# Performance work log

Hardware: AMD Instinct MI355X
Metric: run time of the kernel (lower is better)

Reference implementation:

```python
import jax, jax.numpy as jnp
import numpy as np

N = 50000
E = 1600000
IN_CH = 34
HID = 64
OUT = 64
NEG_SLOPE = 0.2


def _gat_layer(x, src, dst, W, a_src, a_dst, bias, heads, out_ch, concat):
    n = x.shape[0]
    xw = (x @ W).reshape(n, heads, out_ch)                      # [N,H,C]
    al_src = jnp.sum(xw * a_src[None], axis=-1)                  # [N,H]
    al_dst = jnp.sum(xw * a_dst[None], axis=-1)                  # [N,H]
    e = jax.nn.leaky_relu(al_src[src] + al_dst[dst], NEG_SLOPE)  # [E,H]
    # segment softmax over incoming edges of each dst node (self-loops ensure non-empty)
    m = jax.ops.segment_max(e, dst, num_segments=n)              # [N,H]
    ex = jnp.exp(e - m[dst])
    denom = jax.ops.segment_sum(ex, dst, num_segments=n)         # [N,H]
    alpha = ex / denom[dst]                                      # [E,H]
    msg = xw[src] * alpha[:, :, None]                            # [E,H,C]
    out = jax.ops.segment_sum(msg, dst, num_segments=n)          # [N,H,C]
    if concat:
        out = out.reshape(n, heads * out_ch)
    else:
        out = out.mean(axis=1)
    return out + bias


def setup_inputs() -> dict:
    key = jax.random.key(0)
    ks = jax.random.split(key, 12)
    x = jax.random.normal(ks[0], (N, IN_CH), dtype=jnp.float32)
    edge_index = jax.random.randint(ks[1], (2, E), 0, N, dtype=jnp.int64)
    # layer 1: heads=2, concat -> 128
    W1 = jax.random.normal(ks[2], (IN_CH, 2 * HID), dtype=jnp.float32) * 0.1
    a_src1 = jax.random.normal(ks[3], (2, HID), dtype=jnp.float32) * 0.1
    a_dst1 = jax.random.normal(ks[4], (2, HID), dtype=jnp.float32) * 0.1
    b1 = jnp.zeros((2 * HID,), dtype=jnp.float32)
    # layer 2: heads=1, mean
    W2 = jax.random.normal(ks[5], (2 * HID, OUT), dtype=jnp.float32) * 0.1
    a_src2 = jax.random.normal(ks[6], (1, OUT), dtype=jnp.float32) * 0.1
    a_dst2 = jax.random.normal(ks[7], (1, OUT), dtype=jnp.float32) * 0.1
    b2 = jnp.zeros((OUT,), dtype=jnp.float32)
    return {"x": x, "edge_index": edge_index, "W1": W1, "a_src1": a_src1,
            "a_dst1": a_dst1, "b1": b1, "W2": W2, "a_src2": a_src2,
            "a_dst2": a_dst2, "b2": b2}


def reference(x, edge_index, W1, a_src1, a_dst1, b1, W2, a_src2, a_dst2, b2):
    n = x.shape[0]
    loops = jnp.arange(n, dtype=edge_index.dtype)
    src = jnp.concatenate([edge_index[0], loops])  # PyG GATConv add_self_loops=True
    dst = jnp.concatenate([edge_index[1], loops])
    h = _gat_layer(x, src, dst, W1, a_src1, a_dst1, b1, heads=2, out_ch=HID, concat=True)
    h = jax.nn.relu(h)
    out = _gat_layer(h, src, dst, W2, a_src2, a_dst2, b2, heads=1, out_ch=OUT, concat=False)
    return out
```

## Files before the change

### kernel.cpp

```cpp
#include <hip/hip_runtime.h>
#include <math.h>

#define N_NODES 50000
#define E_EDGES 1600000
#define IN_CH   34
#define NEG     0.2f
#define NB      196
#define CAP     10000

typedef __attribute__((ext_vector_type(2))) float fv2;

static __device__ __forceinline__ unsigned short f2bf(float f) {
    unsigned int u = __float_as_uint(f);
    u += 0x7fffu + ((u >> 16) & 1u);
    return (unsigned short)(u >> 16);
}
static __device__ __forceinline__ float bflo(unsigned int u) {
    return __uint_as_float(u << 16);
}
static __device__ __forceinline__ float bfhi(unsigned int u) {
    return __uint_as_float(u & 0xffff0000u);
}
static __device__ __forceinline__ float lrelu_exp(float e) {
    return expf(e > 0.f ? e : NEG * e);
}

static __device__ __forceinline__ int scan256_excl(int v, int* wsum) {
    const int lane = threadIdx.x & 63, wv = threadIdx.x >> 6;
    int x = v;
    #pragma unroll
    for (int off = 1; off < 64; off <<= 1) {
        int y = __shfl_up(x, off);
        if (lane >= off) x += y;
    }
    if (lane == 63) wsum[wv] = x;
    __syncthreads();
    if (threadIdx.x < 4) {
        int s = wsum[threadIdx.x];
        #pragma unroll
        for (int off = 1; off < 4; off <<= 1) {
            int y = __shfl_up(s, off);
            if ((int)threadIdx.x >= off) s += y;
        }
        wsum[threadIdx.x] = s;
    }
    __syncthreads();
    const int woff = wv ? wsum[wv - 1] : 0;
    return woff + x - v;
}

__global__ __launch_bounds__(256) void k_bin_node1(
    const int* __restrict__ srcA, const int* __restrict__ dstA,
    int* __restrict__ gcur, unsigned int* __restrict__ binned,
    const float* __restrict__ x, const float* __restrict__ W1,
    const float* __restrict__ a_src, const float* __restrict__ a_dst,
    unsigned short* __restrict__ xw1b,
    float* __restrict__ al_s, float* __restrict__ al_d)
{
    __shared__ __align__(16) char sm[69664];
    const int tid = threadIdx.x;

    if (blockIdx.x < NB) {
        unsigned int* raw  = (unsigned int*)sm;
        unsigned int* ebuf = (unsigned int*)(sm + 32768);
        int* cnt  = (int*)(sm + 65536);
        int* loff = (int*)(sm + 66560);
        int* lcur = (int*)(sm + 67584);
        int* cur  = (int*)(sm + 68608);
        int* wsum = (int*)(sm + 69632);
        cnt[tid] = 0;
        __syncthreads();
        const int base = blockIdx.x * 8192;
        #pragma unroll
        for (int i = 0; i < 32; ++i) {
            const int e = base + i * 256 + tid;
            if (e < E_EDGES) {
                const int d = dstA[e], s = srcA[e];
                raw[i * 256 + tid] = ((unsigned int)d << 16) | (unsigned int)s;
                atomicAdd(&cnt[d >> 8], 1);
            }
        }
        __syncthreads();
        const int v = cnt[tid];
        const int excl = scan256_excl(v, wsum);
        loff[tid] = excl;
        lcur[tid] = excl;
        cur[tid] = (tid < NB && v > 0) ? (tid * CAP + atomicAdd(&gcur[tid], v)) : 0;
        __syncthreads();
        const int mE = min(8192, E_EDGES - base);
        #pragma unroll
        for (int i = 0; i < 32; ++i) {
            const int p = i * 256 + tid;
            if (p < mE) {
                const unsigned int u = raw[p];
                const int q = atomicAdd(&lcur[u >> 24], 1);
                ebuf[q] = u;
            }
        }
        __syncthreads();
        #pragma unroll
        for (int i = 0; i < 32; ++i) {
            const int p = i * 256 + tid;
            if (p < mE) {
                const unsigned int u = ebuf[p];
                const int b = (int)(u >> 24);
                binned[cur[b] + (p - loff[b])] = u;
            }
        }
    } else {
        float* sW  = (float*)sm;
        float* sx  = (float*)(sm + 17952);
        float* sas = (float*)(sm + 22432);
        float* sad = (float*)(sm + 22944);
        for (int i = tid; i < IN_CH * 128; i += 256) {
            int k = i >> 7, c = i & 127;
            sW[k * 132 + c] = W1[i];
        }
        if (tid < 128) { sas[tid] = a_src[tid]; sad[tid] = a_dst[tid]; }
        const int n0 = (blockIdx.x - NB) * 32;
        for (int i = tid; i < 32 * IN_CH; i += 256) {
            int n = i / IN_CH;
            sx[n * 35 + (i - n * IN_CH)] = (n0 + n < N_NODES) ? x[n0 * IN_CH + i] : 0.f;
        }
        __syncthreads();

        const int tc = tid & 31, tn = tid >> 5;
        float acc[4][4] = {{0.f}};
        for (int k = 0; k < IN_CH; ++k) {
            const float4 wv = *reinterpret_cast<const float4*>(&sW[k * 132 + 4 * tc]);
            #pragma unroll
            for (int j = 0; j < 4; ++j) {
                const float hj = sx[(4 * tn + j) * 35 + k];
                acc[j][0] += hj * wv.x; acc[j][1] += hj * wv.y;
                acc[j][2] += hj * wv.z; acc[j][3] += hj * wv.w;
            }
        }
        #pragma unroll
        for (int j = 0; j < 4; ++j) {
            const int node = n0 + 4 * tn + j;
            float ps = 0.f, pd = 0.f;
            #pragma unroll
            for (int c = 0; c < 4; ++c) {
                ps += acc[j][c] * sas[4 * tc + c];
                pd += acc[j][c] * sad[4 * tc + c];
            }
            #pragma unroll
            for (int off = 1; off < 16; off <<= 1) {
                ps += __shfl_xor(ps, off);
                pd += __shfl_xor(pd, off);
            }
            if (node < N_NODES) {
                if ((tc & 15) == 0) {
                    int h = tc >> 4;
                    al_s[node * 2 + h] = ps;
                    al_d[node * 2 + h] = pd;
                }
                ushort4 u;
                u.x = f2bf(acc[j][0]); u.y = f2bf(acc[j][1]);
                u.z = f2bf(acc[j][2]); u.w = f2bf(acc[j][3]);
                *reinterpret_cast<ushort4*>(&xw1b[node * 128 + 4 * tc]) = u;
            }
        }
    }
}

__global__ __launch_bounds__(256) void k_fine(
    const int* __restrict__ gcur, const unsigned int* __restrict__ binned,
    int2* __restrict__ rowspan, int* __restrict__ sorted_src)
{
    __shared__ unsigned int sbin[CAP];
    __shared__ int cnt[256], lcur[256];
    __shared__ int wsum[4];
    const int tid = threadIdx.x;
    const int b = blockIdx.x;
    const int bbase = b * CAP;
    const int cntb = gcur[b];
    cnt[tid] = 0;
    __syncthreads();
    for (int p = tid; p < cntb; p += 256) {
        const unsigned int u = binned[bbase + p];
        sbin[p] = u;
        atomicAdd(&cnt[(u >> 16) & 255], 1);
    }
    __syncthreads();
    const int v = cnt[tid];
    const int excl = scan256_excl(v, wsum);
    const int node = b * 256 + tid;
    if (node < N_NODES) rowspan[node] = make_int2(bbase + excl, bbase + excl + v);
    lcur[tid] = excl;
    __syncthreads();
    for (int p = tid; p < cntb; p += 256) {
        const unsigned int u = sbin[p];
        const int q = atomicAdd(&lcur[(u >> 16) & 255], 1);
        sorted_src[bbase + q] = (int)(u & 0xffffu);
    }
}

__global__ __launch_bounds__(256) void k_gather1(
    const int2* __restrict__ rowspan, const int* __restrict__ sorted_src,
    const unsigned int* __restrict__ xw1u,
    const float* __restrict__ al_s, const float* __restrict__ al_d,
    const float* __restrict__ b1, float* __restrict__ hbuf)
{
    __shared__ float4 AB[2][4][32];
    const int wave = threadIdx.x >> 6;
    const int lane = threadIdx.x & 63;
    const int node = (blockIdx.x * 256 + threadIdx.x) >> 6;
    if (node >= N_NODES) return;
    const int2 span = rowspan[node];
    const int head = lane >> 5;

    const float2 ald  = *reinterpret_cast<const float2*>(&al_d[node * 2]);
    const float2 als0 = *reinterpret_cast<const float2*>(&al_s[node * 2]);
    const float w0h0 = lrelu_exp(als0.x + ald.x);
    const float w0h1 = lrelu_exp(als0.y + ald.y);
    const float wself = head ? w0h1 : w0h0;

    const unsigned int su = xw1u[node * 64 + lane];
    fv2 accX = { wself * bflo(su), wself * bfhi(su) };
    fv2 accY = { 0.f, 0.f };
    float dv0 = 0.f, dv1 = 0.f;
    const float4* ABh = AB[head][wave];

    for (int base = span.x; base < span.y; base += 64) {
        const int rem = span.y - base;
        const int m = rem < 64 ? rem : 64;
        const int mp = (m + 1) & ~1;
        if (lane < m) {
            const int s = sorted_src[base + lane];
            const float2 als = *reinterpret_cast<const float2*>(&al_s[s * 2]);
            const float w0 = lrelu_exp(als.x + ald.x);
            const float w1 = lrelu_exp(als.y + ald.y);
            dv0 += w0; dv1 += w1;
            const float offf = __int_as_float(s << 6);
            ((float2*)&AB[0][wave][lane >> 1])[lane & 1] = make_float2(offf, w0);
            ((float2*)&AB[1][wave][lane >> 1])[lane & 1] = make_float2(offf, w1);
        } else if (lane < mp) {
            const float offf = __int_as_float(node << 6);
            ((float2*)&AB[0][wave][lane >> 1])[lane & 1] = make_float2(offf, 0.f);
            ((float2*)&AB[1][wave][lane >> 1])[lane & 1] = make_float2(offf, 0.f);
        }
        const int P = mp >> 1;
        int p = 0;
        for (; p + 4 <= P; p += 4) {
            const float4 q0 = ABh[p + 0];
            const float4 q1 = ABh[p + 1];
            const float4 q2 = ABh[p + 2];
            const float4 q3 = ABh[p + 3];
            const unsigned int a0 = xw1u[__float_as_int(q0.x) + lane];
            const unsigned int b0 = xw1u[__float_as_int(q0.z) + lane];
            const unsigned int a1 = xw1u[__float_as_int(q1.x) + lane];
            const unsigned int b1v = xw1u[__float_as_int(q1.z) + lane];
            const unsigned int a2 = xw1u[__float_as_int(q2.x) + lane];
            const unsigned int b2 = xw1u[__float_as_int(q2.z) + lane];
            const unsigned int a3 = xw1u[__float_as_int(q3.x) + lane];
            const unsigned int b3 = xw1u[__float_as_int(q3.z) + lane];
            fv2 f;
            f.x = bflo(a0); f.y = bfhi(a0); accX += f * q0.y;
            f.x = bflo(b0); f.y = bfhi(b0); accY += f * q0.w;
            f.x = bflo(a1); f.y = bfhi(a1); accX += f * q1.y;
            f.x = bflo(b1v); f.y = bfhi(b1v); accY += f * q1.w;
            f.x = bflo(a2); f.y = bfhi(a2); accX += f * q2.y;
            f.x = bflo(b2); f.y = bfhi(b2); accY += f * q2.w;
            f.x = bflo(a3); f.y = bfhi(a3); accX += f * q3.y;
            f.x = bflo(b3); f.y = bfhi(b3); accY += f * q3.w;
        }
        for (; p < P; ++p) {
            const float4 q = ABh[p];
            const unsigned int a = xw1u[__float_as_int(q.x) + lane];
            const unsigned int b = xw1u[__float_as_int(q.z) + lane];
            fv2 f;
            f.x = bflo(a); f.y = bfhi(a); accX += f * q.y;
            f.x = bflo(b); f.y = bfhi(b); accY += f * q.w;
        }
    }
    accX += accY;
    #pragma unroll
    for (int off = 32; off; off >>= 1) {
        dv0 += __shfl_xor(dv0, off);
        dv1 += __shfl_xor(dv1, off);
    }
    const float den = head ? (dv1 + w0h1) : (dv0 + w0h0);
    const float2 bv = *reinterpret_cast<const float2*>(&b1[2 * lane]);
    float o0 = accX.x / den + bv.x;
    float o1 = accX.y / den + bv.y;
    o0 = o0 > 0.f ? o0 : 0.f;
    o1 = o1 > 0.f ? o1 : 0.f;
    *reinterpret_cast<float2*>(&hbuf[node * 128 + 2 * lane]) = make_float2(o0, o1);
}

__global__ __launch_bounds__(256) void k_node2(
    const float* __restrict__ hbuf, const float* __restrict__ W2,
    const float* __restrict__ a_src, const float* __restrict__ a_dst,
    unsigned short* __restrict__ xw2b, float* __restrict__ al_s, float* __restrict__ al_d)
{
    __shared__ float sW[128 * 64];
    __shared__ float sh[64 * 129];
    __shared__ float sas[64], sad[64];
    const int tid = threadIdx.x;
    for (int i = tid; i < 128 * 64; i += 256) sW[i] = W2[i];
    if (tid < 64) { sas[tid] = a_src[tid]; sad[tid] = a_dst[tid]; }
    const int n0 = blockIdx.x * 64;
    for (int i = tid; i < 64 * 128; i += 256) {
        int n = i >> 7, c = i & 127;
        sh[n * 129 + c] = (n0 + n < N_NODES) ? hbuf[(long)(n0 + n) * 128 + c] : 0.f;
    }
    __syncthreads();

    const int tc = tid & 15, tn = tid >> 4;
    float acc[4][4] = {{0.f}};
    for (int k = 0; k < 128; ++k) {
        const float4 wv = *reinterpret_cast<const float4*>(&sW[k * 64 + 4 * tc]);
        #pragma unroll
        for (int j = 0; j < 4; ++j) {
            const float hj = sh[(4 * tn + j) * 129 + k];
            acc[j][0] += hj * wv.x; acc[j][1] += hj * wv.y;
            acc[j][2] += hj * wv.z; acc[j][3] += hj * wv.w;
        }
    }
    #pragma unroll
    for (int j = 0; j < 4; ++j) {
        const int node = n0 + 4 * tn + j;
        float ps = 0.f, pd = 0.f;
        #pragma unroll
        for (int c = 0; c < 4; ++c) {
            ps += acc[j][c] * sas[4 * tc + c];
            pd += acc[j][c] * sad[4 * tc + c];
        }
        #pragma unroll
        for (int off = 1; off < 16; off <<= 1) {
            ps += __shfl_xor(ps, off);
            pd += __shfl_xor(pd, off);
        }
        if (node < N_NODES) {
            if (tc == 0) { al_s[node] = ps; al_d[node] = pd; }
            ushort4 u;
            u.x = f2bf(acc[j][0]); u.y = f2bf(acc[j][1]);
            u.z = f2bf(acc[j][2]); u.w = f2bf(acc[j][3]);
            *reinterpret_cast<ushort4*>(&xw2b[node * 64 + 4 * tc]) = u;
        }
    }
}

__global__ __launch_bounds__(256) void k_gather2(
    const int2* __restrict__ rowspan, const int* __restrict__ sorted_src,
    const unsigned int* __restrict__ xw2u,
    const float* __restrict__ al_s, const float* __restrict__ al_d,
    const float* __restrict__ b2, float* __restrict__ out)
{
    __shared__ float4 AB[4][32];
    const int wave = threadIdx.x >> 6;
    const int lane = threadIdx.x & 63;
    const int node = (blockIdx.x * 256 + threadIdx.x) >> 6;
    if (node >= N_NODES) return;
    const int2 span = rowspan[node];
    const int li = lane & 31, hsel = lane >> 5;

    const float ald = al_d[node];
    const float w0s = lrelu_exp(al_s[node] + ald);
    const unsigned int su = xw2u[node * 32 + li];
    const float wself = hsel ? 0.f : w0s;
    fv2 acc = { wself * bflo(su), wself * bfhi(su) };
    float dv = 0.f;
    const float4* ABw = AB[wave];

    for (int base = span.x; base < span.y; base += 64) {
        const int rem = span.y - base;
        const int m = rem < 64 ? rem : 64;
        const int mp = (m + 3) & ~3;
        if (lane < m) {
            const int s = sorted_src[base + lane];
            const float w = lrelu_exp(al_s[s] + ald);
            dv += w;
            ((float2*)&AB[wave][lane >> 1])[lane & 1] =
                make_float2(__int_as_float(s << 5), w);
        } else if (lane < mp) {
            ((float2*)&AB[wave][lane >> 1])[lane & 1] =
                make_float2(__int_as_float(node << 5), 0.f);
        }
        const int P = mp >> 1;
        int p = hsel;
        for (; p + 2 < P; p += 4) {
            const float4 qA = ABw[p];
            const float4 qB = ABw[p + 2];
            const unsigned int aA = xw2u[__float_as_int(qA.x) + li];
            const unsigned int bA = xw2u[__float_as_int(qA.z) + li];
            const unsigned int aB = xw2u[__float_as_int(qB.x) + li];
            const unsigned int bB = xw2u[__float_as_int(qB.z) + li];
            fv2 f;
            f.x = bflo(aA); f.y = bfhi(aA); acc += f * qA.y;
            f.x = bflo(bA); f.y = bfhi(bA); acc += f * qA.w;
            f.x = bflo(aB); f.y = bfhi(aB); acc += f * qB.y;
            f.x = bflo(bB); f.y = bfhi(bB); acc += f * qB.w;
        }
        for (; p < P; p += 2) {
            const float4 q = ABw[p];
            const unsigned int a = xw2u[__float_as_int(q.x) + li];
            const unsigned int b = xw2u[__float_as_int(q.z) + li];
            fv2 f;
            f.x = bflo(a); f.y = bfhi(a); acc += f * q.y;
            f.x = bflo(b); f.y = bfhi(b); acc += f * q.w;
        }
    }
    acc.x += __shfl_xor(acc.x, 32);
    acc.y += __shfl_xor(acc.y, 32);
    #pragma unroll
    for (int off = 32; off; off >>= 1) dv += __shfl_xor(dv, off);
    if (lane < 32) {
        const float den = dv + w0s;
        const float2 bv = *reinterpret_cast<const float2*>(&b2[2 * li]);
        *reinterpret_cast<float2*>(&out[node * 64 + 2 * li]) =
            make_float2(acc.x / den + bv.x, acc.y / den + bv.y);
    }
}

extern "C" void kernel_launch(void* const* d_in, const int* in_sizes, int n_in,
                              void* d_out, int out_size, void* d_ws, size_t ws_size,
                              hipStream_t stream)
{
    const float* x   = (const float*)d_in[0];
    const int*   ei  = (const int*)d_in[1];
    const float* W1  = (const float*)d_in[2];
    const float* as1 = (const float*)d_in[3];
    const float* ad1 = (const float*)d_in[4];
    const float* b1  = (const float*)d_in[5];
    const float* W2  = (const float*)d_in[6];
    const float* as2 = (const float*)d_in[7];
    const float* ad2 = (const float*)d_in[8];
    const float* b2  = (const float*)d_in[9];
    float* out = (float*)d_out;

    const int* srcA = ei;
    const int* dstA = ei + E_EDGES;

    char* ws = (char*)d_ws;
    int2*  rowspan    = (int2*)(ws);
    int*   sorted_src = (int*)(ws + 409600);
    int*   gcur       = (int*)(ws + 8249600);
    float* al_s1      = (float*)(ws + 8251648);
    float* al_d1      = (float*)(ws + 8651648);
    float* al_s2      = (float*)(ws + 9051648);
    float* al_d2      = (float*)(ws + 9251648);
    unsigned short* xw1b = (unsigned short*)(ws + 9451648);
    float* hbuf       = (float*)(ws + 22251648);
    unsigned int* binned = (unsigned int*)hbuf;
    unsigned short* xw2b = (unsigned short*)(ws + 47851648);

    hipMemsetAsync(gcur, 0, NB * sizeof(int), stream);
    hipLaunchKernelGGL(k_bin_node1, dim3(NB + (N_NODES + 31) / 32), dim3(256), 0, stream,
                       srcA, dstA, gcur, binned,
                       x, W1, as1, ad1, xw1b, al_s1, al_d1);
    hipLaunchKernelGGL(k_fine, dim3(NB), dim3(256), 0, stream,
                       gcur, binned, rowspan, sorted_src);
    hipLaunchKernelGGL(k_gather1, dim3((N_NODES + 3) / 4), dim3(256), 0, stream,
                       rowspan, sorted_src, (const unsigned int*)xw1b,
                       al_s1, al_d1, b1, hbuf);
    hipLaunchKernelGGL(k_node2, dim3((N_NODES + 63) / 64), dim3(256), 0, stream,
                       hbuf, W2, as2, ad2, xw2b, al_s2, al_d2);
    hipLaunchKernelGGL(k_gather2, dim3((N_NODES + 3) / 4), dim3(256), 0, stream,
                       rowspan, sorted_src, (const unsigned int*)xw2b,
                       al_s2, al_d2, b2, out);
}
```

Before: 268.2 us.

## Fuse layer-2 projection into gather1, split binning, use ranks and 16-bit source indices

Layer 2's linear projection and attention logits now run inside k_gather1. Each wave multiplies its node's relu output by a bf16-packed W2 held in shared memory, so the fp32 hidden buffer and the separate k_node2 kernel are gone. The binning and fine-sort kernels record per-edge ranks from the counting atomics, which removes the second atomic pass and the local reorder buffer; the binning kernel also moves to smaller 4096-edge blocks and is split from the layer-1 node transform. Sorted source indices shrink to uint16 to cut gather traffic, and W2 in bf16 adds rounding error. Every gather1 block now reloads 16KB of W2 from global memory into shared memory, and the grids assume N is divisible by 4.

```diff
diff --git a/kernel.cpp b/kernel.cpp
--- a/kernel.cpp
+++ b/kernel.cpp
@@ -49,127 +49,44 @@
     return woff + x - v;
 }
 
-__global__ __launch_bounds__(256) void k_bin_node1(
+__global__ __launch_bounds__(256) void k_bin(
     const int* __restrict__ srcA, const int* __restrict__ dstA,
-    int* __restrict__ gcur, unsigned int* __restrict__ binned,
-    const float* __restrict__ x, const float* __restrict__ W1,
-    const float* __restrict__ a_src, const float* __restrict__ a_dst,
-    unsigned short* __restrict__ xw1b,
-    float* __restrict__ al_s, float* __restrict__ al_d)
-{
-    __shared__ __align__(16) char sm[69664];
+    int* __restrict__ gcur, unsigned int* __restrict__ binned)
+{
+    __shared__ unsigned int raw[4096];
+    __shared__ unsigned short rnk[4096];
+    __shared__ int cnt[256], cur[256];
     const int tid = threadIdx.x;
-
-    if (blockIdx.x < NB) {
-        unsigned int* raw  = (unsigned int*)sm;
-        unsigned int* ebuf = (unsigned int*)(sm + 32768);
-        int* cnt  = (int*)(sm + 65536);
-        int* loff = (int*)(sm + 66560);
-        int* lcur = (int*)(sm + 67584);
-        int* cur  = (int*)(sm + 68608);
-        int* wsum = (int*)(sm + 69632);
-        cnt[tid] = 0;
-        __syncthreads();
-        const int base = blockIdx.x * 8192;
-        #pragma unroll
-        for (int i = 0; i < 32; ++i) {
-            const int e = base + i * 256 + tid;
-            if (e < E_EDGES) {
-                const int d = dstA[e], s = srcA[e];
-                raw[i * 256 + tid] = ((unsigned int)d << 16) | (unsigned int)s;
-                atomicAdd(&cnt[d >> 8], 1);
-            }
-        }
-        __syncthreads();
-        const int v = cnt[tid];
-        const int excl = scan256_excl(v, wsum);
-        loff[tid] = excl;
-        lcur[tid] = excl;
-        cur[tid] = (tid < NB && v > 0) ? (tid * CAP + atomicAdd(&gcur[tid], v)) : 0;
-        __syncthreads();
-        const int mE = min(8192, E_EDGES - base);
-        #pragma unroll
-        for (int i = 0; i < 32; ++i) {
-            const int p = i * 256 + tid;
-            if (p < mE) {
-                const unsigned int u = raw[p];
-                const int q = atomicAdd(&lcur[u >> 24], 1);
-                ebuf[q] = u;
-            }
-        }
-        __syncthreads();
-        #pragma unroll
-        for (int i = 0; i < 32; ++i) {
-            const int p = i * 256 + tid;
-            if (p < mE) {
-                const unsigned int u = ebuf[p];
-                const int b = (int)(u >> 24);
-                binned[cur[b] + (p - loff[b])] = u;
-            }
-        }
-    } else {
-        float* sW  = (float*)sm;
-        float* sx  = (float*)(sm + 17952);
-        float* sas = (float*)(sm + 22432);
-        float* sad = (float*)(sm + 22944);
-        for (int i = tid; i < IN_CH * 128; i += 256) {
-            int k = i >> 7, c = i & 127;
-            sW[k * 132 + c] = W1[i];
-        }
-        if (tid < 128) { sas[tid] = a_src[tid]; sad[tid] = a_dst[tid]; }
-        const int n0 = (blockIdx.x - NB) * 32;
-        for (int i = tid; i < 32 * IN_CH; i += 256) {
-            int n = i / IN_CH;
-            sx[n * 35 + (i - n * IN_CH)] = (n0 + n < N_NODES) ? x[n0 * IN_CH + i] : 0.f;
-        }
-        __syncthreads();
-
-        const int tc = tid & 31, tn = tid >> 5;
-        float acc[4][4] = {{0.f}};
-        for (int k = 0; k < IN_CH; ++k) {
-            const float4 wv = *reinterpret_cast<const float4*>(&sW[k * 132 + 4 * tc]);
-            #pragma unroll
-            for (int j = 0; j < 4; ++j) {
-                const float hj = sx[(4 * tn + j) * 35 + k];
-                acc[j][0] += hj * wv.x; acc[j][1] += hj * wv.y;
-                acc[j][2] += hj * wv.z; acc[j][3] += hj * wv.w;
-            }
-        }
-        #pragma unroll
-        for (int j = 0; j < 4; ++j) {
-            const int node = n0 + 4 * tn + j;
-            float ps = 0.f, pd = 0.f;
-            #pragma unroll
-            for (int c = 0; c < 4; ++c) {
-                ps += acc[j][c] * sas[4 * tc + c];
-                pd += acc[j][c] * sad[4 * tc + c];
-            }
-            #pragma unroll
-            for (int off = 1; off < 16; off <<= 1) {
-                ps += __shfl_xor(ps, off);
-                pd += __shfl_xor(pd, off);
-            }
-            if (node < N_NODES) {
-                if ((tc & 15) == 0) {
-                    int h = tc >> 4;
-                    al_s[node * 2 + h] = ps;
-                    al_d[node * 2 + h] = pd;
-                }
-                ushort4 u;
-                u.x = f2bf(acc[j][0]); u.y = f2bf(acc[j][1]);
-                u.z = f2bf(acc[j][2]); u.w = f2bf(acc[j][3]);
-                *reinterpret_cast<ushort4*>(&xw1b[node * 128 + 4 * tc]) = u;
-            }
-        }
+    cnt[tid] = 0;
+    __syncthreads();
+    const int base = blockIdx.x * 4096;
+    #pragma unroll
+    for (int i = 0; i < 16; ++i) {
+        const int e = base + i * 256 + tid;
+        if (e < E_EDGES) {
+            const int d = dstA[e], s = srcA[e];
+            raw[i * 256 + tid] = ((unsigned int)d << 16) | (unsigned int)s;
+            rnk[i * 256 + tid] = (unsigned short)atomicAdd(&cnt[d >> 8], 1);
+        }
+    }
+    __syncthreads();
+    const int v = cnt[tid];
+    cur[tid] = (tid < NB && v > 0) ? (tid * CAP + atomicAdd(&gcur[tid], v)) : 0;
+    __syncthreads();
+    const int mE = min(4096, E_EDGES - base);
+    for (int p = tid; p < mE; p += 256) {
+        const unsigned int u = raw[p];
+        binned[cur[u >> 24] + rnk[p]] = u;
     }
 }
 
 __global__ __launch_bounds__(256) void k_fine(
     const int* __restrict__ gcur, const unsigned int* __restrict__ binned,
-    int2* __restrict__ rowspan, int* __restrict__ sorted_src)
+    int2* __restrict__ rowspan, unsigned short* __restrict__ sorted_src)
 {
     __shared__ unsigned int sbin[CAP];
-    __shared__ int cnt[256], lcur[256];
+    __shared__ unsigned short rnk[CAP];
+    __shared__ int cnt[256], sbase[256];
     __shared__ int wsum[4];
     const int tid = threadIdx.x;
     const int b = blockIdx.x;
@@ -180,33 +97,111 @@
     for (int p = tid; p < cntb; p += 256) {
         const unsigned int u = binned[bbase + p];
         sbin[p] = u;
-        atomicAdd(&cnt[(u >> 16) & 255], 1);
+        rnk[p] = (unsigned short)atomicAdd(&cnt[(u >> 16) & 255], 1);
     }
     __syncthreads();
     const int v = cnt[tid];
     const int excl = scan256_excl(v, wsum);
     const int node = b * 256 + tid;
     if (node < N_NODES) rowspan[node] = make_int2(bbase + excl, bbase + excl + v);
-    lcur[tid] = excl;
+    sbase[tid] = excl;
     __syncthreads();
     for (int p = tid; p < cntb; p += 256) {
         const unsigned int u = sbin[p];
-        const int q = atomicAdd(&lcur[(u >> 16) & 255], 1);
-        sorted_src[bbase + q] = (int)(u & 0xffffu);
+        sorted_src[bbase + sbase[(u >> 16) & 255] + rnk[p]] =
+            (unsigned short)(u & 0xffffu);
+    }
+}
+
+__global__ __launch_bounds__(256) void k_node1(
+    const float* __restrict__ x, const float* __restrict__ W1,
+    const float* __restrict__ a_src, const float* __restrict__ a_dst,
+    unsigned short* __restrict__ xw1b,
+    float* __restrict__ al_s, float* __restrict__ al_d,
+    const float* __restrict__ W2, unsigned int* __restrict__ w2p)
+{
+    __shared__ float sW[IN_CH * 132];
+    __shared__ float sx[32 * 35];
+    __shared__ float sas[128], sad[128];
+    const int tid = threadIdx.x;
+    if (blockIdx.x == 0) {
+        for (int i = tid; i < 4096; i += 256) {
+            const int k2 = i >> 6, c = i & 63;
+            const unsigned int lo = f2bf(W2[(2 * k2) * 64 + c]);
+            const unsigned int hi = f2bf(W2[(2 * k2 + 1) * 64 + c]);
+            w2p[i] = lo | (hi << 16);
+        }
+    }
+    for (int i = tid; i < IN_CH * 128; i += 256) {
+        int k = i >> 7, c = i & 127;
+        sW[k * 132 + c] = W1[i];
+    }
+    if (tid < 128) { sas[tid] = a_src[tid]; sad[tid] = a_dst[tid]; }
+    const int n0 = blockIdx.x * 32;
+    for (int i = tid; i < 32 * IN_CH; i += 256) {
+        int n = i / IN_CH;
+        sx[n * 35 + (i - n * IN_CH)] = (n0 + n < N_NODES) ? x[n0 * IN_CH + i] : 0.f;
+    }
+    __syncthreads();
+
+    const int tc = tid & 31, tn = tid >> 5;
+    float acc[4][4] = {{0.f}};
+    for (int k = 0; k < IN_CH; ++k) {
+        const float4 wv = *reinterpret_cast<const float4*>(&sW[k * 132 + 4 * tc]);
+        #pragma unroll
+        for (int j = 0; j < 4; ++j) {
+            const float hj = sx[(4 * tn + j) * 35 + k];
+            acc[j][0] += hj * wv.x; acc[j][1] += hj * wv.y;
+            acc[j][2] += hj * wv.z; acc[j][3] += hj * wv.w;
+        }
+    }
+    #pragma unroll
+    for (int j = 0; j < 4; ++j) {
+        const int node = n0 + 4 * tn + j;
+        float ps = 0.f, pd = 0.f;
+        #pragma unroll
+        for (int c = 0; c < 4; ++c) {
+            ps += acc[j][c] * sas[4 * tc + c];
+            pd += acc[j][c] * sad[4 * tc + c];
+        }
+        #pragma unroll
+        for (int off = 1; off < 16; off <<= 1) {
+            ps += __shfl_xor(ps, off);
+            pd += __shfl_xor(pd, off);
+        }
+        if (node < N_NODES) {
+            if ((tc & 15) == 0) {
+                int h = tc >> 4;
+                al_s[node * 2 + h] = ps;
+                al_d[node * 2 + h] = pd;
+            }
+            ushort4 u;
+            u.x = f2bf(acc[j][0]); u.y = f2bf(acc[j][1]);
+            u.z = f2bf(acc[j][2]); u.w = f2bf(acc[j][3]);
+            *reinterpret_cast<ushort4*>(&xw1b[node * 128 + 4 * tc]) = u;
+        }
     }
 }
 
 __global__ __launch_bounds__(256) void k_gather1(
-    const int2* __restrict__ rowspan, const int* __restrict__ sorted_src,
+    const int2* __restrict__ rowspan, const unsigned short* __restrict__ sorted_src,
     const unsigned int* __restrict__ xw1u,
     const float* __restrict__ al_s, const float* __restrict__ al_d,
-    const float* __restrict__ b1, float* __restrict__ hbuf)
-{
+    const float* __restrict__ b1, const unsigned int* __restrict__ w2p,
+    const float* __restrict__ as2, const float* __restrict__ ad2,
+    unsigned short* __restrict__ xw2b,
+    float* __restrict__ al_s2, float* __restrict__ al_d2)
+{
+    __shared__ unsigned int sW2[4096];
     __shared__ float4 AB[2][4][32];
-    const int wave = threadIdx.x >> 6;
-    const int lane = threadIdx.x & 63;
-    const int node = (blockIdx.x * 256 + threadIdx.x) >> 6;
-    if (node >= N_NODES) return;
+    __shared__ float2 sh2[4][64];
+    const int tid = threadIdx.x;
+    for (int i = tid; i < 4096; i += 256) sW2[i] = w2p[i];
+    __syncthreads();
+
+    const int wave = tid >> 6;
+    const int lane = tid & 63;
+    const int node = blockIdx.x * 4 + wave;
     const int2 span = rowspan[node];
     const int head = lane >> 5;
 
@@ -286,64 +281,28 @@
     float o1 = accX.y / den + bv.y;
     o0 = o0 > 0.f ? o0 : 0.f;
     o1 = o1 > 0.f ? o1 : 0.f;
-    *reinterpret_cast<float2*>(&hbuf[node * 128 + 2 * lane]) = make_float2(o0, o1);
-}
-
-__global__ __launch_bounds__(256) void k_node2(
-    const float* __restrict__ hbuf, const float* __restrict__ W2,
-    const float* __restrict__ a_src, const float* __restrict__ a_dst,
-    unsigned short* __restrict__ xw2b, float* __restrict__ al_s, float* __restrict__ al_d)
-{
-    __shared__ float sW[128 * 64];
-    __shared__ float sh[64 * 129];
-    __shared__ float sas[64], sad[64];
-    const int tid = threadIdx.x;
-    for (int i = tid; i < 128 * 64; i += 256) sW[i] = W2[i];
-    if (tid < 64) { sas[tid] = a_src[tid]; sad[tid] = a_dst[tid]; }
-    const int n0 = blockIdx.x * 64;
-    for (int i = tid; i < 64 * 128; i += 256) {
-        int n = i >> 7, c = i & 127;
-        sh[n * 129 + c] = (n0 + n < N_NODES) ? hbuf[(long)(n0 + n) * 128 + c] : 0.f;
-    }
-    __syncthreads();
-
-    const int tc = tid & 15, tn = tid >> 4;
-    float acc[4][4] = {{0.f}};
-    for (int k = 0; k < 128; ++k) {
-        const float4 wv = *reinterpret_cast<const float4*>(&sW[k * 64 + 4 * tc]);
-        #pragma unroll
-        for (int j = 0; j < 4; ++j) {
-            const float hj = sh[(4 * tn + j) * 129 + k];
-            acc[j][0] += hj * wv.x; acc[j][1] += hj * wv.y;
-            acc[j][2] += hj * wv.z; acc[j][3] += hj * wv.w;
-        }
-    }
-    #pragma unroll
-    for (int j = 0; j < 4; ++j) {
-        const int node = n0 + 4 * tn + j;
-        float ps = 0.f, pd = 0.f;
-        #pragma unroll
-        for (int c = 0; c < 4; ++c) {
-            ps += acc[j][c] * sas[4 * tc + c];
-            pd += acc[j][c] * sad[4 * tc + c];
-        }
-        #pragma unroll
-        for (int off = 1; off < 16; off <<= 1) {
-            ps += __shfl_xor(ps, off);
-            pd += __shfl_xor(pd, off);
-        }
-        if (node < N_NODES) {
-            if (tc == 0) { al_s[node] = ps; al_d[node] = pd; }
-            ushort4 u;
-            u.x = f2bf(acc[j][0]); u.y = f2bf(acc[j][1]);
-            u.z = f2bf(acc[j][2]); u.w = f2bf(acc[j][3]);
-            *reinterpret_cast<ushort4*>(&xw2b[node * 64 + 4 * tc]) = u;
-        }
-    }
+
+    sh2[wave][lane] = make_float2(o0, o1);
+    float a2acc = 0.f;
+    #pragma unroll 4
+    for (int k2 = 0; k2 < 64; ++k2) {
+        const float2 hp = sh2[wave][k2];
+        const unsigned int wv2 = sW2[k2 * 64 + lane];
+        a2acc += hp.x * bflo(wv2) + hp.y * bfhi(wv2);
+    }
+    float ps2 = a2acc * as2[lane];
+    float pd2 = a2acc * ad2[lane];
+    #pragma unroll
+    for (int off = 32; off; off >>= 1) {
+        ps2 += __shfl_xor(ps2, off);
+        pd2 += __shfl_xor(pd2, off);
+    }
+    xw2b[node * 64 + lane] = f2bf(a2acc);
+    if (lane == 0) { al_s2[node] = ps2; al_d2[node] = pd2; }
 }
 
 __global__ __launch_bounds__(256) void k_gather2(
-    const int2* __restrict__ rowspan, const int* __restrict__ sorted_src,
+    const int2* __restrict__ rowspan, const unsigned short* __restrict__ sorted_src,
     const unsigned int* __restrict__ xw2u,
     const float* __restrict__ al_s, const float* __restrict__ al_d,
     const float* __restrict__ b2, float* __restrict__ out)
@@ -351,8 +310,7 @@
     __shared__ float4 AB[4][32];
     const int wave = threadIdx.x >> 6;
     const int lane = threadIdx.x & 63;
-    const int node = (blockIdx.x * 256 + threadIdx.x) >> 6;
-    if (node >= N_NODES) return;
+    const int node = blockIdx.x * 4 + wave;
     const int2 span = rowspan[node];
     const int li = lane & 31, hsel = lane >> 5;
 
@@ -434,30 +392,29 @@
     const int* dstA = ei + E_EDGES;
 
     char* ws = (char*)d_ws;
-    int2*  rowspan    = (int2*)(ws);
-    int*   sorted_src = (int*)(ws + 409600);
-    int*   gcur       = (int*)(ws + 8249600);
-    float* al_s1      = (float*)(ws + 8251648);
-    float* al_d1      = (float*)(ws + 8651648);
-    float* al_s2      = (float*)(ws + 9051648);
-    float* al_d2      = (float*)(ws + 9251648);
-    unsigned short* xw1b = (unsigned short*)(ws + 9451648);
-    float* hbuf       = (float*)(ws + 22251648);
-    unsigned int* binned = (unsigned int*)hbuf;
-    unsigned short* xw2b = (unsigned short*)(ws + 47851648);
+    int2*           rowspan    = (int2*)(ws);
+    unsigned short* sorted_src = (unsigned short*)(ws + 409600);
+    int*            gcur       = (int*)(ws + 4341760);
+    float*          al_s1      = (float*)(ws + 4343808);
+    float*          al_d1      = (float*)(ws + 4753408);
+    float*          al_s2      = (float*)(ws + 5163008);
+    float*          al_d2      = (float*)(ws + 5367808);
+    unsigned short* xw1b       = (unsigned short*)(ws + 5572608);
+    unsigned int*   binned     = (unsigned int*)(ws + 18376704);
+    unsigned short* xw2b       = (unsigned short*)(ws + 26220544);
+    unsigned int*   w2p        = (unsigned int*)(ws + 32620544);
 
     hipMemsetAsync(gcur, 0, NB * sizeof(int), stream);
-    hipLaunchKernelGGL(k_bin_node1, dim3(NB + (N_NODES + 31) / 32), dim3(256), 0, stream,
-                       srcA, dstA, gcur, binned,
-                       x, W1, as1, ad1, xw1b, al_s1, al_d1);
+    hipLaunchKernelGGL(k_bin, dim3((E_EDGES + 4095) / 4096), dim3(256), 0, stream,
+                       srcA, dstA, gcur, binned);
+    hipLaunchKernelGGL(k_node1, dim3((N_NODES + 31) / 32), dim3(256), 0, stream,
+                       x, W1, as1, ad1, xw1b, al_s1, al_d1, W2, w2p);
     hipLaunchKernelGGL(k_fine, dim3(NB), dim3(256), 0, stream,
                        gcur, binned, rowspan, sorted_src);
-    hipLaunchKernelGGL(k_gather1, dim3((N_NODES + 3) / 4), dim3(256), 0, stream,
+    hipLaunchKernelGGL(k_gather1, dim3(N_NODES / 4), dim3(256), 0, stream,
                        rowspan, sorted_src, (const unsigned int*)xw1b,
-                       al_s1, al_d1, b1, hbuf);
-    hipLaunchKernelGGL(k_node2, dim3((N_NODES + 63) / 64), dim3(256), 0, stream,
-                       hbuf, W2, as2, ad2, xw2b, al_s2, al_d2);
-    hipLaunchKernelGGL(k_gather2, dim3((N_NODES + 3) / 4), dim3(256), 0, stream,
+                       al_s1, al_d1, b1, w2p, as2, ad2, xw2b, al_s2, al_d2);
+    hipLaunchKernelGGL(k_gather2, dim3(N_NODES / 4), dim3(256), 0, stream,
                        rowspan, sorted_src, (const unsigned int*)xw2b,
                        al_s2, al_d2, b2, out);
 }
```

New measurement: 272.9 us. No clear change (+1.7%).
